# Optimization experiments

Hardware: AMD Instinct MI355X
Metric: run time of the kernel (lower is better)

Reference implementation:

```python
import jax, jax.numpy as jnp
import numpy as np

M, N = 4096, 4096


def _makhoul_perm(n):
    # Makhoul even/odd reordering: v[k] = x[2k] for k < ceil(n/2),
    # v[n-1-k] = x[2k+1] for the rest. This is the same input permutation
    # the dct2_fft2 kernel applies before its rfft2.
    idx = np.empty(n, dtype=np.int32)
    half = (n + 1) // 2
    idx[:half] = 2 * np.arange(half)
    idx[half:] = 2 * (n - 1 - np.arange(half, n)) + 1
    return jnp.asarray(idx)


def _dct2_1d_last(x):
    # Unnormalized DCT-II along the last axis via a same-length FFT plus
    # twiddle (expk) multiply:  C[k] = Re( exp(-i*pi*k/(2n)) * FFT(v)[k] )
    # which equals sum_m x[m] * cos(pi*k*(2m+1)/(2n)).
    n = x.shape[-1]
    v = jnp.take(x, _makhoul_perm(n), axis=-1)
    V = jnp.fft.fft(v, axis=-1)
    k = jnp.arange(n)
    expk = jnp.exp((-1j * np.pi / (2.0 * n)) * k)  # twiddle factors (expkM/expkN)
    return jnp.real(V * expk).astype(x.dtype)


def setup_inputs() -> dict:
    key = jax.random.key(0)
    x = jax.random.normal(key, (M, N), dtype=jnp.float32)
    return {"x": x}


def reference(x):
    # Separable 2D DCT-II: along axis -1 (uses expkN), then axis -2 (expkM).
    y = _dct2_1d_last(x)        # DCT over columns index (length N)
    y = _dct2_1d_last(y.T).T    # DCT over rows index (length M)
    return y
```

## Files before the change

### kernel.cpp

```cpp
#include <hip/hip_runtime.h>
#include <stdint.h>


#define NF 4096

__device__ __forceinline__ int physi(int e) { return e ^ ((e >> 4) & 15); }

__device__ __forceinline__ float2 cadd(float2 a, float2 b) {
    float2 r; r.x = a.x + b.x; r.y = a.y + b.y; return r;
}
__device__ __forceinline__ float2 csub(float2 a, float2 b) {
    float2 r; r.x = a.x - b.x; r.y = a.y - b.y; return r;
}
__device__ __forceinline__ float2 cmulc(float2 a, float2 b) {
    float2 r; r.x = a.x * b.x - a.y * b.y; r.y = a.x * b.y + a.y * b.x; return r;
}
__device__ __forceinline__ float2 rotm(float2 a) {
    float2 r; r.x = a.y; r.y = -a.x; return r;
}

__global__ __launch_bounds__(256) void setup_tables(float* __restrict__ tw,
                                                    float* __restrict__ ek) {
    int idx = blockIdx.x * 256 + threadIdx.x;
    if (idx < 4416) {
        int p, u; float denom;
        if (idx < 64)       { p = idx >> 3;         u = idx & 7;  denom = 64.0f; }
        else if (idx < 320) { int r = idx - 64;  p = r >> 4; u = r & 15; denom = 256.0f; }
        else                { int r = idx - 320; p = r >> 4; u = r & 15; denom = 4096.0f; }
        float phi = (float)(p * u) * (6.283185307179586f / denom);
        float s, c; __sincosf(phi, &s, &c);
        tw[2 * idx]     = c;
        tw[2 * idx + 1] = -s;
    } else if (idx < 8512) {
        int k = idx - 4416;
        float th = (float)k * (3.141592653589793f / 8192.0f);
        float s, c; __sincosf(th, &s, &c);
        ek[2 * k]     = c;
        ek[2 * k + 1] = s;
    }
}

#define RADIX8(Xv, E0, E1, E2, E3, O0, g1, g2, g3)                             \
    float2 t0 = cadd(Xv[0], Xv[4]), t1 = csub(Xv[0], Xv[4]);                   \
    float2 t2 = cadd(Xv[2], Xv[6]), t3 = csub(Xv[2], Xv[6]);                   \
    float2 E0 = cadd(t0, t2), E2 = csub(t0, t2);                               \
    float2 r3 = rotm(t3);                                                      \
    float2 E1 = cadd(t1, r3), E3 = csub(t1, r3);                               \
    float2 s0 = cadd(Xv[1], Xv[5]), s1 = csub(Xv[1], Xv[5]);                   \
    float2 s2 = cadd(Xv[3], Xv[7]), s3 = csub(Xv[3], Xv[7]);                   \
    float2 O0 = cadd(s0, s2), O2 = csub(s0, s2);                               \
    float2 r7 = rotm(s3);                                                      \
    float2 O1 = cadd(s1, r7), O3 = csub(s1, r7);                               \
    const float SQ = 0.7071067811865476f;                                      \
    float2 g1; g1.x = SQ * (O1.x + O1.y); g1.y = SQ * (O1.y - O1.x);           \
    float2 g2 = rotm(O2);                                                      \
    float2 g3; g3.x = SQ * (O3.y - O3.x); g3.y = -SQ * (O3.x + O3.y);

__device__ __forceinline__ void dft16(float2* x) {
    float2 E[8], O[8];
    {
        float2 a[8];
        #pragma unroll
        for (int m = 0; m < 8; ++m) a[m] = x[2 * m];
        RADIX8(a, E0, E1, E2, E3, O0, g1, g2, g3)
        E[0] = cadd(E0, O0); E[1] = cadd(E1, g1);
        E[2] = cadd(E2, g2); E[3] = cadd(E3, g3);
        E[4] = csub(E0, O0); E[5] = csub(E1, g1);
        E[6] = csub(E2, g2); E[7] = csub(E3, g3);
    }
    {
        float2 a[8];
        #pragma unroll
        for (int m = 0; m < 8; ++m) a[m] = x[2 * m + 1];
        RADIX8(a, E0, E1, E2, E3, O0, g1, g2, g3)
        O[0] = cadd(E0, O0); O[1] = cadd(E1, g1);
        O[2] = cadd(E2, g2); O[3] = cadd(E3, g3);
        O[4] = csub(E0, O0); O[5] = csub(E1, g1);
        O[6] = csub(E2, g2); O[7] = csub(E3, g3);
    }
    const float2 W1 = { 0.9238795325112867f, -0.3826834323650898f};
    const float2 W2 = { 0.7071067811865476f, -0.7071067811865476f};
    const float2 W3 = { 0.3826834323650898f, -0.9238795325112867f};
    const float2 W5 = {-0.3826834323650898f, -0.9238795325112867f};
    const float2 W6 = {-0.7071067811865476f, -0.7071067811865476f};
    const float2 W7 = {-0.9238795325112867f, -0.3826834323650898f};
    float2 t;
    x[0] = cadd(E[0], O[0]);  x[8]  = csub(E[0], O[0]);
    t = cmulc(O[1], W1); x[1] = cadd(E[1], t); x[9]  = csub(E[1], t);
    t = cmulc(O[2], W2); x[2] = cadd(E[2], t); x[10] = csub(E[2], t);
    t = cmulc(O[3], W3); x[3] = cadd(E[3], t); x[11] = csub(E[3], t);
    t = rotm(O[4]);      x[4] = cadd(E[4], t); x[12] = csub(E[4], t);
    t = cmulc(O[5], W5); x[5] = cadd(E[5], t); x[13] = csub(E[5], t);
    t = cmulc(O[6], W6); x[6] = cadd(E[6], t); x[14] = csub(E[6], t);
    t = cmulc(O[7], W7); x[7] = cadd(E[7], t); x[15] = csub(E[7], t);
}

__global__ __launch_bounds__(256) void dct_rows(const float* __restrict__ In,
                                                float* __restrict__ Out,
                                                const float* __restrict__ tw,
                                                const float* __restrict__ ek) {
    __shared__ float2 buf[NF];
    const int j = threadIdx.x;
    const int b = blockIdx.x;
    const float* in0 = In + (size_t)(2 * b) * NF;
    const float* in1 = in0 + NF;
    float* out0 = Out + (size_t)b * NF;
    float* out1 = Out + (size_t)(4095 - b) * NF;

    float2 x[16];

    #pragma unroll
    for (int k = 0; k < 16; ++k) {
        int n = j + 256 * k;
        int idx = (n < 2048) ? (2 * n) : (8191 - 2 * n);
        x[k].x = in0[idx];
        x[k].y = in1[idx];
    }
    dft16(x);
    #pragma unroll
    for (int i = 0; i < 16; ++i)
        buf[physi(16 * j + i)] = x[i];
    __syncthreads();

    {
        const int p = j & 15, q = j >> 4;
        #pragma unroll
        for (int k = 0; k < 16; ++k)
            x[k] = buf[physi(j + 256 * k)];
        const float2* twp = (const float2*)tw + 64 + p * 16;
        #pragma unroll
        for (int k = 1; k < 16; ++k)
            x[k] = cmulc(x[k], twp[k]);
        dft16(x);
        __syncthreads();
        int wb = p + 256 * q;
        #pragma unroll
        for (int i = 0; i < 16; ++i)
            buf[physi(wb + 16 * i)] = x[i];
        __syncthreads();
    }

    {
        #pragma unroll
        for (int k = 0; k < 16; ++k)
            x[k] = buf[physi(j + 256 * k)];
        const float2* twp = (const float2*)tw + 320 + j * 16;
        #pragma unroll
        for (int k = 1; k < 16; ++k)
            x[k] = cmulc(x[k], twp[k]);
        dft16(x);
        #pragma unroll
        for (int i = 0; i < 16; ++i)
            buf[physi(j + 256 * i)] = x[i];
    }
    __syncthreads();

    #pragma unroll
    for (int i = 0; i < 16; ++i) {
        int k = j + 256 * i;
        int m = (NF - k) & (NF - 1);
        float2 Zk = x[i];
        float2 Zm = buf[physi(m)];
        float2 E = ((const float2*)ek)[k];
        out0[k] = 0.5f * ((Zk.x + Zm.x) * E.x + (Zk.y - Zm.y) * E.y);
        out1[k] = 0.5f * ((Zk.y + Zm.y) * E.x - (Zk.x - Zm.x) * E.y);
    }
}

__global__ __launch_bounds__(256) void col_fft1(const float* __restrict__ V,
                                                float* __restrict__ S,
                                                const float* __restrict__ tw) {
    __shared__ float2 T[64][32];
    __shared__ float2 w64[64];
    const int ct = blockIdx.x, n1 = blockIdx.y;
    const int t = threadIdx.x;
    const int cp = t & 31, j = t >> 5;
    const float2* inb = (const float2*)V + (size_t)ct * 32 + cp;

    if (t < 64) {
        int m = (n1 * t) & 4095;
        float phi = (float)m * -1.5339807878856412e-3f;
        float s, c; __sincosf(phi, &s, &c);
        float2 w; w.x = c; w.y = s;
        w64[t] = w;
    }

    float2 x[8];
    #pragma unroll
    for (int k = 0; k < 8; ++k) {
        int row = n1 + 64 * (j + 8 * k);
        x[k] = inb[(size_t)row * 2048];
    }
    {
        RADIX8(x, E0, E1, E2, E3, O0, g1, g2, g3)
        T[8 * j + 0][cp] = cadd(E0, O0);
        T[8 * j + 1][cp] = cadd(E1, g1);
        T[8 * j + 2][cp] = cadd(E2, g2);
        T[8 * j + 3][cp] = cadd(E3, g3);
        T[8 * j + 4][cp] = csub(E0, O0);
        T[8 * j + 5][cp] = csub(E1, g1);
        T[8 * j + 6][cp] = csub(E2, g2);
        T[8 * j + 7][cp] = csub(E3, g3);
    }
    __syncthreads();

    float2 o[8];
    {
        #pragma unroll
        for (int k = 0; k < 8; ++k)
            x[k] = T[j + 8 * k][cp];
        const float2* twp = (const float2*)tw + j * 8;
        #pragma unroll
        for (int k = 1; k < 8; ++k)
            x[k] = cmulc(x[k], twp[k]);
        RADIX8(x, E0, E1, E2, E3, O0, g1, g2, g3)
        o[0] = cadd(E0, O0); o[1] = cadd(E1, g1);
        o[2] = cadd(E2, g2); o[3] = cadd(E3, g3);
        o[4] = csub(E0, O0); o[5] = csub(E1, g1);
        o[6] = csub(E2, g2); o[7] = csub(E3, g3);
    }

    float2* outb = (float2*)S + (size_t)ct * 32 + cp;
    #pragma unroll
    for (int i = 0; i < 8; ++i) {
        int k2 = j + 8 * i;
        float2 h = cmulc(o[i], w64[k2]);
        outb[(size_t)(64 * k2 + n1) * 2048] = h;
    }
}

__global__ __launch_bounds__(512) void col_fft2(const float* __restrict__ S,
                                                float* __restrict__ Out,
                                                const float* __restrict__ tw,
                                                const float* __restrict__ ek) {
    __shared__ float2 T[2][64][32];
    const int ct = blockIdx.x, bp = blockIdx.y;
    const int ga = bp, gb = (bp == 0) ? 32 : 64 - bp;
    const int t = threadIdx.x;
    const int cp = t & 31, j = (t >> 5) & 7, gi = t >> 8;
    const int g = gi ? gb : ga;
    const float2* inb = (const float2*)S + (size_t)ct * 32 + cp;

    float2 x[8];
    #pragma unroll
    for (int k = 0; k < 8; ++k)
        x[k] = inb[(size_t)(64 * g + j + 8 * k) * 2048];
    {
        RADIX8(x, E0, E1, E2, E3, O0, g1, g2, g3)
        T[gi][8 * j + 0][cp] = cadd(E0, O0);
        T[gi][8 * j + 1][cp] = cadd(E1, g1);
        T[gi][8 * j + 2][cp] = cadd(E2, g2);
        T[gi][8 * j + 3][cp] = cadd(E3, g3);
        T[gi][8 * j + 4][cp] = csub(E0, O0);
        T[gi][8 * j + 5][cp] = csub(E1, g1);
        T[gi][8 * j + 6][cp] = csub(E2, g2);
        T[gi][8 * j + 7][cp] = csub(E3, g3);
    }
    __syncthreads();

    float2 o[8];
    {
        #pragma unroll
        for (int k = 0; k < 8; ++k)
            x[k] = T[gi][j + 8 * k][cp];
        const float2* twp = (const float2*)tw + j * 8;
        #pragma unroll
        for (int k = 1; k < 8; ++k)
            x[k] = cmulc(x[k], twp[k]);
        RADIX8(x, E0, E1, E2, E3, O0, g1, g2, g3)
        o[0] = cadd(E0, O0); o[1] = cadd(E1, g1);
        o[2] = cadd(E2, g2); o[3] = cadd(E3, g3);
        o[4] = csub(E0, O0); o[5] = csub(E1, g1);
        o[6] = csub(E2, g2); o[7] = csub(E3, g3);
        #pragma unroll
        for (int i = 0; i < 8; ++i)
            T[gi][j + 8 * i][cp] = o[i];
    }
    __syncthreads();

    float2* outb = (float2*)Out + (size_t)ct * 32 + cp;
    #pragma unroll
    for (int i = 0; i < 8; ++i) {
        int k = 64 * (j + 8 * i) + g;
        int m = (NF - k) & (NF - 1);
        int gp = m & 63, k1p = m >> 6;
        float2 Zk = o[i];
        float2 Zm = T[(gp == ga) ? 0 : 1][k1p][cp];
        float2 E = ((const float2*)ek)[k];
        float2 r;
        r.x = 0.5f * ((Zk.x + Zm.x) * E.x + (Zk.y - Zm.y) * E.y);
        r.y = 0.5f * ((Zk.y + Zm.y) * E.x - (Zk.x - Zm.x) * E.y);
        outb[(size_t)k * 2048] = r;
    }
}

extern "C" void kernel_launch(void* const* d_in, const int* in_sizes, int n_in,
                              void* d_out, int out_size, void* d_ws, size_t ws_size,
                              hipStream_t stream) {
    const float* x = (const float*)d_in[0];
    float* out = (float*)d_out;

    float* tw = (float*)d_ws;
    float* ek = tw + 8832;
    float* B1 = ek + 8192;
    if (ws_size < (size_t)68096 + (size_t)NF * NF * sizeof(float)) return;

    setup_tables<<<34, 256, 0, stream>>>(tw, ek);
    dct_rows<<<NF / 2, 256, 0, stream>>>(x, out, tw, ek);
    col_fft1<<<dim3(64, 64), 256, 0, stream>>>(out, B1, tw);
    col_fft2<<<dim3(64, 32), 512, 0, stream>>>(B1, out, tw, ek);
}
```

Measured before the change: 169.0 us.

## Vectorize global loads in row DCT and column FFT pass one

In dct_rows, the strided scalar gather that applies the Makhoul permutation is replaced by coalesced float4 loads of both input rows. The values are scattered into shared memory in permuted order, which costs an extra barrier. In col_fft1, each thread now handles two adjacent columns through float4 global loads and stores, so the grid is halved and the shared tile doubled. The aim is wider, better-coalesced memory transactions, at the cost of more registers and shared memory per block.

```diff
diff --git a/kernel.cpp b/kernel.cpp
--- a/kernel.cpp
+++ b/kernel.cpp
@@ -56,27 +56,28 @@
     float2 g2 = rotm(O2);                                                      \
     float2 g3; g3.x = SQ * (O3.y - O3.x); g3.y = -SQ * (O3.x + O3.y);
 
+#define RADIX8_OUT(Xv, Ov)                                                     \
+    {                                                                          \
+        RADIX8(Xv, E0, E1, E2, E3, O0, g1, g2, g3)                             \
+        Ov[0] = cadd(E0, O0); Ov[1] = cadd(E1, g1);                            \
+        Ov[2] = cadd(E2, g2); Ov[3] = cadd(E3, g3);                            \
+        Ov[4] = csub(E0, O0); Ov[5] = csub(E1, g1);                            \
+        Ov[6] = csub(E2, g2); Ov[7] = csub(E3, g3);                            \
+    }
+
 __device__ __forceinline__ void dft16(float2* x) {
     float2 E[8], O[8];
     {
         float2 a[8];
         #pragma unroll
         for (int m = 0; m < 8; ++m) a[m] = x[2 * m];
-        RADIX8(a, E0, E1, E2, E3, O0, g1, g2, g3)
-        E[0] = cadd(E0, O0); E[1] = cadd(E1, g1);
-        E[2] = cadd(E2, g2); E[3] = cadd(E3, g3);
-        E[4] = csub(E0, O0); E[5] = csub(E1, g1);
-        E[6] = csub(E2, g2); E[7] = csub(E3, g3);
+        RADIX8_OUT(a, E)
     }
     {
         float2 a[8];
         #pragma unroll
         for (int m = 0; m < 8; ++m) a[m] = x[2 * m + 1];
-        RADIX8(a, E0, E1, E2, E3, O0, g1, g2, g3)
-        O[0] = cadd(E0, O0); O[1] = cadd(E1, g1);
-        O[2] = cadd(E2, g2); O[3] = cadd(E3, g3);
-        O[4] = csub(E0, O0); O[5] = csub(E1, g1);
-        O[6] = csub(E2, g2); O[7] = csub(E3, g3);
+        RADIX8_OUT(a, O)
     }
     const float2 W1 = { 0.9238795325112867f, -0.3826834323650898f};
     const float2 W2 = { 0.7071067811865476f, -0.7071067811865476f};
@@ -107,16 +108,31 @@
     float* out0 = Out + (size_t)b * NF;
     float* out1 = Out + (size_t)(4095 - b) * NF;
 
+    const float4* i40 = (const float4*)in0;
+    const float4* i41 = (const float4*)in1;
+    #pragma unroll
+    for (int c = 0; c < 4; ++c) {
+        float4 a0 = i40[j + 256 * c];
+        float4 a1 = i41[j + 256 * c];
+        int nb = 2 * j + 512 * c;
+        float2 z0; z0.x = a0.x; z0.y = a1.x;
+        float2 z1; z1.x = a0.z; z1.y = a1.z;
+        float2 z2; z2.x = a0.y; z2.y = a1.y;
+        float2 z3; z3.x = a0.w; z3.y = a1.w;
+        buf[physi(nb)]        = z0;
+        buf[physi(nb + 1)]    = z1;
+        buf[physi(4095 - nb)] = z2;
+        buf[physi(4094 - nb)] = z3;
+    }
+    __syncthreads();
+
     float2 x[16];
 
     #pragma unroll
-    for (int k = 0; k < 16; ++k) {
-        int n = j + 256 * k;
-        int idx = (n < 2048) ? (2 * n) : (8191 - 2 * n);
-        x[k].x = in0[idx];
-        x[k].y = in1[idx];
-    }
+    for (int k = 0; k < 16; ++k)
+        x[k] = buf[physi(j + 256 * k)];
     dft16(x);
+    __syncthreads();
     #pragma unroll
     for (int i = 0; i < 16; ++i)
         buf[physi(16 * j + i)] = x[i];
@@ -170,12 +186,12 @@
 __global__ __launch_bounds__(256) void col_fft1(const float* __restrict__ V,
                                                 float* __restrict__ S,
                                                 const float* __restrict__ tw) {
-    __shared__ float2 T[64][32];
+    __shared__ float2 T[64][64];
     __shared__ float2 w64[64];
     const int ct = blockIdx.x, n1 = blockIdx.y;
     const int t = threadIdx.x;
-    const int cp = t & 31, j = t >> 5;
-    const float2* inb = (const float2*)V + (size_t)ct * 32 + cp;
+    const int cp4 = t & 31, j = t >> 5;
+    const float4* in4 = (const float4*)V + (size_t)ct * 32 + cp4;
 
     if (t < 64) {
         int m = (n1 * t) & 4095;
@@ -185,47 +201,51 @@
         w64[t] = w;
     }
 
-    float2 x[8];
+    float2 xA[8], xB[8];
     #pragma unroll
     for (int k = 0; k < 8; ++k) {
-        int row = n1 + 64 * (j + 8 * k);
-        x[k] = inb[(size_t)row * 2048];
-    }
-    {
-        RADIX8(x, E0, E1, E2, E3, O0, g1, g2, g3)
-        T[8 * j + 0][cp] = cadd(E0, O0);
-        T[8 * j + 1][cp] = cadd(E1, g1);
-        T[8 * j + 2][cp] = cadd(E2, g2);
-        T[8 * j + 3][cp] = cadd(E3, g3);
-        T[8 * j + 4][cp] = csub(E0, O0);
-        T[8 * j + 5][cp] = csub(E1, g1);
-        T[8 * j + 6][cp] = csub(E2, g2);
-        T[8 * j + 7][cp] = csub(E3, g3);
-    }
-    __syncthreads();
-
-    float2 o[8];
-    {
-        #pragma unroll
-        for (int k = 0; k < 8; ++k)
-            x[k] = T[j + 8 * k][cp];
+        float4 v4 = in4[(size_t)(n1 + 64 * (j + 8 * k)) * 1024];
+        xA[k].x = v4.x; xA[k].y = v4.y;
+        xB[k].x = v4.z; xB[k].y = v4.w;
+    }
+    {
+        float2 rA[8], rB[8];
+        RADIX8_OUT(xA, rA)
+        RADIX8_OUT(xB, rB)
+        #pragma unroll
+        for (int i = 0; i < 8; ++i) {
+            float4 w; w.x = rA[i].x; w.y = rA[i].y; w.z = rB[i].x; w.w = rB[i].y;
+            *(float4*)&T[8 * j + i][2 * cp4] = w;
+        }
+    }
+    __syncthreads();
+
+    float2 oA[8], oB[8];
+    {
+        #pragma unroll
+        for (int k = 0; k < 8; ++k) {
+            float4 v4 = *(const float4*)&T[j + 8 * k][2 * cp4];
+            xA[k].x = v4.x; xA[k].y = v4.y;
+            xB[k].x = v4.z; xB[k].y = v4.w;
+        }
         const float2* twp = (const float2*)tw + j * 8;
         #pragma unroll
-        for (int k = 1; k < 8; ++k)
-            x[k] = cmulc(x[k], twp[k]);
-        RADIX8(x, E0, E1, E2, E3, O0, g1, g2, g3)
-        o[0] = cadd(E0, O0); o[1] = cadd(E1, g1);
-        o[2] = cadd(E2, g2); o[3] = cadd(E3, g3);
-        o[4] = csub(E0, O0); o[5] = csub(E1, g1);
-        o[6] = csub(E2, g2); o[7] = csub(E3, g3);
-    }
-
-    float2* outb = (float2*)S + (size_t)ct * 32 + cp;
+        for (int k = 1; k < 8; ++k) {
+            xA[k] = cmulc(xA[k], twp[k]);
+            xB[k] = cmulc(xB[k], twp[k]);
+        }
+        RADIX8_OUT(xA, oA)
+        RADIX8_OUT(xB, oB)
+    }
+
+    float4* out4 = (float4*)S + (size_t)ct * 32 + cp4;
     #pragma unroll
     for (int i = 0; i < 8; ++i) {
         int k2 = j + 8 * i;
-        float2 h = cmulc(o[i], w64[k2]);
-        outb[(size_t)(64 * k2 + n1) * 2048] = h;
+        float2 hA = cmulc(oA[i], w64[k2]);
+        float2 hB = cmulc(oB[i], w64[k2]);
+        float4 w; w.x = hA.x; w.y = hA.y; w.z = hB.x; w.w = hB.y;
+        out4[(size_t)(64 * k2 + n1) * 1024] = w;
     }
 }
 
@@ -246,15 +266,11 @@
     for (int k = 0; k < 8; ++k)
         x[k] = inb[(size_t)(64 * g + j + 8 * k) * 2048];
     {
-        RADIX8(x, E0, E1, E2, E3, O0, g1, g2, g3)
-        T[gi][8 * j + 0][cp] = cadd(E0, O0);
-        T[gi][8 * j + 1][cp] = cadd(E1, g1);
-        T[gi][8 * j + 2][cp] = cadd(E2, g2);
-        T[gi][8 * j + 3][cp] = cadd(E3, g3);
-        T[gi][8 * j + 4][cp] = csub(E0, O0);
-        T[gi][8 * j + 5][cp] = csub(E1, g1);
-        T[gi][8 * j + 6][cp] = csub(E2, g2);
-        T[gi][8 * j + 7][cp] = csub(E3, g3);
+        float2 r[8];
+        RADIX8_OUT(x, r)
+        #pragma unroll
+        for (int i = 0; i < 8; ++i)
+            T[gi][8 * j + i][cp] = r[i];
     }
     __syncthreads();
 
@@ -267,11 +283,7 @@
         #pragma unroll
         for (int k = 1; k < 8; ++k)
             x[k] = cmulc(x[k], twp[k]);
-        RADIX8(x, E0, E1, E2, E3, O0, g1, g2, g3)
-        o[0] = cadd(E0, O0); o[1] = cadd(E1, g1);
-        o[2] = cadd(E2, g2); o[3] = cadd(E3, g3);
-        o[4] = csub(E0, O0); o[5] = csub(E1, g1);
-        o[6] = csub(E2, g2); o[7] = csub(E3, g3);
+        RADIX8_OUT(x, o)
         #pragma unroll
         for (int i = 0; i < 8; ++i)
             T[gi][j + 8 * i][cp] = o[i];
@@ -307,6 +319,6 @@
 
     setup_tables<<<34, 256, 0, stream>>>(tw, ek);
     dct_rows<<<NF / 2, 256, 0, stream>>>(x, out, tw, ek);
-    col_fft1<<<dim3(64, 64), 256, 0, stream>>>(out, B1, tw);
+    col_fft1<<<dim3(32, 64), 256, 0, stream>>>(out, B1, tw);
     col_fft2<<<dim3(64, 32), 512, 0, stream>>>(B1, out, tw, ek);
 }
```

New measurement: 167.6 us. Within noise of the previous version (-0.9%).
